# Kernel optimization log

Hardware: AMD Instinct MI355X
Metric: run time of the kernel (lower is better)

The kernel has to match this reference:

```python
import jax, jax.numpy as jnp
import numpy as np

B, S, D, H = 2, 2048, 1024, 16
HD = D // H  # head_dim = 64


def setup_inputs() -> dict:
    key = jax.random.key(0)
    ks = jax.random.split(key, 9)
    sc = 1.0 / np.sqrt(D)
    return {
        "X": jax.random.normal(ks[0], (B, S, D), jnp.float32),
        "Wq": jax.random.normal(ks[1], (D, D), jnp.float32) * sc,
        "bq": jnp.zeros((D,), jnp.float32),
        "Wk": jax.random.normal(ks[2], (D, D), jnp.float32) * sc,
        "bk": jnp.zeros((D,), jnp.float32),
        "Wv": jax.random.normal(ks[3], (D, D), jnp.float32) * sc,
        "bv": jnp.zeros((D,), jnp.float32),
        "Wo": jax.random.normal(ks[4], (D, D), jnp.float32) * sc,
        "bo": jnp.zeros((D,), jnp.float32),
    }


def reference(X, Wq, bq, Wk, bk, Wv, bv, Wo, bo):
    b, s, d = X.shape
    q = (X @ Wq + bq).reshape(b, s, H, HD).transpose(0, 2, 1, 3)  # [B,H,S,HD]
    k = (X @ Wk + bk).reshape(b, s, H, HD).transpose(0, 2, 1, 3)
    v = (X @ Wv + bv).reshape(b, s, H, HD).transpose(0, 2, 1, 3)
    score = jnp.einsum("bhqd,bhkd->bhqk", q, k) / jnp.sqrt(jnp.float32(HD))
    causal = jnp.tril(jnp.ones((s, s), bool))  # [S,S]
    score = jnp.where(causal[None, None], score, -jnp.inf)
    attn = jax.nn.softmax(score, axis=-1)
    out = jnp.einsum("bhqk,bhkd->bhqd", attn, v)  # [B,H,S,HD]
    out = out.transpose(0, 2, 1, 3).reshape(b, s, d)
    return out @ Wo + bo
```

## Files before the change

kernel.cpp:

```cpp
#include <hip/hip_runtime.h>
#include <hip/hip_bf16.h>
#include <math.h>

#define B_SZ 2
#define S_SZ 2048
#define D_SZ 1024
#define H_SZ 16
#define HD_SZ 64
constexpr int M_ROWS = B_SZ * S_SZ;

typedef __bf16 bf16x8 __attribute__((ext_vector_type(8)));
typedef __bf16 bf16x4 __attribute__((ext_vector_type(4)));
typedef float f32x4 __attribute__((ext_vector_type(4)));

#define GLOAD_LDS16(gsrc, ldst)                                              \
  __builtin_amdgcn_global_load_lds(                                          \
      (const __attribute__((address_space(1))) void*)(gsrc),                 \
      (__attribute__((address_space(3))) void*)(ldst), 16, 0, 0)

__global__ __launch_bounds__(256) void cvt_bf16(const float* __restrict__ in,
                                                __bf16* __restrict__ out,
                                                int n8) {
  const int i = blockIdx.x * 256 + threadIdx.x;
  if (i >= n8) return;
  const float4 a = *reinterpret_cast<const float4*>(&in[i * 8]);
  const float4 b = *reinterpret_cast<const float4*>(&in[i * 8 + 4]);
  bf16x8 o;
  o[0] = (__bf16)a.x; o[1] = (__bf16)a.y; o[2] = (__bf16)a.z; o[3] = (__bf16)a.w;
  o[4] = (__bf16)b.x; o[5] = (__bf16)b.y; o[6] = (__bf16)b.z; o[7] = (__bf16)b.w;
  *reinterpret_cast<bf16x8*>(&out[i * 8]) = o;
}

__global__ __launch_bounds__(256) void cvt_w_t_all(const float* __restrict__ W0,
                                                   const float* __restrict__ W1,
                                                   const float* __restrict__ W2,
                                                   const float* __restrict__ W3,
                                                   __bf16* __restrict__ Wt) {
  __shared__ float Ts[32][33];
  const int z = blockIdx.z;
  const float* W = z == 0 ? W0 : (z == 1 ? W1 : (z == 2 ? W2 : W3));
  __bf16* out = Wt + (size_t)z * 1024 * 1024;
  const int k0 = blockIdx.x * 32, n0 = blockIdx.y * 32;
  const int tr = threadIdx.x >> 3;
  const int tc = (threadIdx.x & 7) * 4;
  const float4 v = *reinterpret_cast<const float4*>(&W[(size_t)(k0 + tr) * 1024 + n0 + tc]);
  Ts[tr][tc + 0] = v.x;
  Ts[tr][tc + 1] = v.y;
  Ts[tr][tc + 2] = v.z;
  Ts[tr][tc + 3] = v.w;
  __syncthreads();
  bf16x4 o;
#pragma unroll
  for (int j = 0; j < 4; ++j) o[j] = (__bf16)Ts[tc + j][tr];
  *reinterpret_cast<bf16x4*>(&out[(size_t)(n0 + tr) * 1024 + k0 + tc]) = o;
}

__global__ __launch_bounds__(256) void transpose_v(const __bf16* __restrict__ V,
                                                   __bf16* __restrict__ Vt) {
  constexpr int TST = 66;
  __shared__ __bf16 T[64 * TST];
  const int bh = blockIdx.y;
  const int s0 = blockIdx.x * 64;
  const size_t base = (size_t)bh * S_SZ * HD_SZ;
  const int tid = threadIdx.x;
  for (int i = tid; i < 512; i += 256) {
    const int r = i >> 3, c = (i & 7) * 8;
    *reinterpret_cast<bf16x8*>(&T[r * TST + c]) =
        *reinterpret_cast<const bf16x8*>(&V[base + (size_t)(s0 + r) * 64 + c]);
  }
  __syncthreads();
  const size_t obase = (size_t)bh * HD_SZ * S_SZ;
  for (int i = tid; i < 512; i += 256) {
    const int d = i >> 3, c = (i & 7) * 8;
    bf16x8 o;
#pragma unroll
    for (int j = 0; j < 8; ++j) o[j] = T[(c + j) * TST + d];
    *reinterpret_cast<bf16x8*>(&Vt[obase + (size_t)d * S_SZ + s0 + c]) = o;
  }
}

template <int MODE>
__global__ __launch_bounds__(256) void gemm_mfma(
    const __bf16* __restrict__ Ab, const __bf16* __restrict__ Bt,
    const float* __restrict__ bias0, const float* __restrict__ bias1,
    const float* __restrict__ bias2, float* __restrict__ C0,
    __bf16* __restrict__ Q0, __bf16* __restrict__ K0, __bf16* __restrict__ V0,
    int M, int N, int K) {
  __shared__ __bf16 As[2][128 * 32];
  __shared__ __bf16 Bs[2][128 * 32];

  const int tid = threadIdx.x;
  const int lane = tid & 63;
  const int w = tid >> 6;
  const int lr = lane & 15, lg = lane >> 4;
  const int wr = w >> 1, wc = w & 1;
  const int bm = blockIdx.x * 128;
  const int bn = blockIdx.y * 128;

  const int r0 = tid >> 2, c0 = (tid & 3) * 8;
  const int r1 = (tid + 256) >> 2, c1 = ((tid + 256) & 3) * 8;
  const __bf16* aS0 = &Ab[(size_t)(bm + r0) * K + c0];
  const __bf16* aS1 = &Ab[(size_t)(bm + r1) * K + c1];
  const __bf16* bS0 = &Bt[(size_t)(bn + r0) * K + c0];
  const __bf16* bS1 = &Bt[(size_t)(bn + r1) * K + c1];

  f32x4 acc[4][4] = {};

  auto STAGE = [&](int buf) {
    GLOAD_LDS16(aS0, &As[buf][w * 512]);
    GLOAD_LDS16(aS1, &As[buf][2048 + w * 512]);
    GLOAD_LDS16(bS0, &Bs[buf][w * 512]);
    GLOAD_LDS16(bS1, &Bs[buf][2048 + w * 512]);
    aS0 += 32; aS1 += 32; bS0 += 32; bS1 += 32;
  };

  STAGE(0);
  asm volatile("s_waitcnt vmcnt(0)" ::: "memory");
  __builtin_amdgcn_s_barrier();
  __builtin_amdgcn_sched_barrier(0);
  int cur = 0;

  for (int k0 = 0; k0 < K; k0 += 32) {
    const bool has_next = (k0 + 32 < K);
    if (has_next) STAGE(cur ^ 1);
    if (k0) {
      if (has_next)
        asm volatile("s_waitcnt vmcnt(4)" ::: "memory");
      else
        asm volatile("s_waitcnt vmcnt(0)" ::: "memory");
      __builtin_amdgcn_s_barrier();
      __builtin_amdgcn_sched_barrier(0);
    }

    bf16x8 af[4], bfr[4];
#pragma unroll
    for (int i = 0; i < 4; ++i)
      af[i] = *reinterpret_cast<const bf16x8*>(&As[cur][(wr * 64 + i * 16 + lr) * 32 + lg * 8]);
#pragma unroll
    for (int j = 0; j < 4; ++j)
      bfr[j] = *reinterpret_cast<const bf16x8*>(&Bs[cur][(wc * 64 + j * 16 + lr) * 32 + lg * 8]);
    __builtin_amdgcn_s_setprio(1);
#pragma unroll
    for (int i = 0; i < 4; ++i)
#pragma unroll
      for (int j = 0; j < 4; ++j)
        acc[i][j] = __builtin_amdgcn_mfma_f32_16x16x32_bf16(af[i], bfr[j], acc[i][j], 0, 0, 0);
    __builtin_amdgcn_s_setprio(0);
    __builtin_amdgcn_sched_barrier(0);
    __builtin_amdgcn_s_barrier();
    cur ^= 1;
  }

  if (MODE == 0) {
#pragma unroll
    for (int j = 0; j < 4; ++j) {
      const int n = bn + wc * 64 + j * 16 + lr;
      const float bs = bias0[n];
#pragma unroll
      for (int i = 0; i < 4; ++i) {
        const int mrow = bm + wr * 64 + i * 16 + lg * 4;
#pragma unroll
        for (int r = 0; r < 4; ++r)
          C0[(size_t)(mrow + r) * N + n] = acc[i][j][r] + bs;
      }
    }
  } else {
    const int which = bn >> 10;
    __bf16* dst = which == 0 ? Q0 : (which == 1 ? K0 : V0);
    const float* bp = which == 0 ? bias0 : (which == 1 ? bias1 : bias2);
    const float scale = which == 0 ? 0.18033688011112042f : 1.0f;
#pragma unroll
    for (int j = 0; j < 4; ++j) {
      const int nn = (bn & 1023) + wc * 64 + j * 16 + lr;
      const int hh = nn >> 6, hd = nn & 63;
      const float bs = bp[nn];
#pragma unroll
      for (int i = 0; i < 4; ++i) {
        const int mrow = bm + wr * 64 + i * 16 + lg * 4;
#pragma unroll
        for (int r = 0; r < 4; ++r) {
          const int m = mrow + r;
          const int bb = m >> 11, ss = m & (S_SZ - 1);
          dst[(((size_t)(bb * H_SZ + hh)) * S_SZ + ss) * HD_SZ + hd] =
              (__bf16)((acc[i][j][r] + bs) * scale);
        }
      }
    }
  }
}

__global__ __launch_bounds__(256) void attn_mfma(const __bf16* __restrict__ Q,
                                                 const __bf16* __restrict__ Kg,
                                                 const __bf16* __restrict__ Vtg,
                                                 __bf16* __restrict__ Aout) {
  constexpr int PST = 40;
  __shared__ __bf16 Ks[2][64 * 64];
  __shared__ __bf16 Vts[2][64 * 64];
  __shared__ __bf16 Ps[4][16 * PST];

  const int tid = threadIdx.x;
  const int lane = tid & 63;
  const int w = tid >> 6;
  const int lr = lane & 15;
  const int lg = lane >> 4;

  const int flat = blockIdx.x;
  const int qb = 31 - (flat >> 5);
  const int hb = flat & 31;
  const int h = hb >> 1, b = hb & 1;
  const size_t base = (size_t)(b * H_SZ + h) * S_SZ * HD_SZ;
  const int q0 = qb * 64 + w * 16;

  bf16x8 aq[2];
#pragma unroll
  for (int hh = 0; hh < 2; ++hh)
    aq[hh] = *reinterpret_cast<const bf16x8*>(
        &Q[base + (size_t)(q0 + lr) * 64 + hh * 32 + lg * 8]);

  const int srow = lane >> 3;
  const int schunk = (lane & 7) ^ srow;

  bf16x8 ones8;
#pragma unroll
  for (int j = 0; j < 8; ++j) ones8[j] = (__bf16)1.0f;

  f32x4 oacc[4] = {};
  f32x4 oacc_l = {};

  const int ntiles = qb + 1;

  const int rbA = w * 16, rbB = w * 16 + 8;
  const __bf16* kS0 = &Kg[base + (size_t)(rbA + srow) * 64 + schunk * 8];
  const __bf16* kS1 = &Kg[base + (size_t)(rbB + srow) * 64 + schunk * 8];
  const __bf16* vS0 = &Vtg[base + (size_t)(rbA + srow) * S_SZ + schunk * 8];
  const __bf16* vS1 = &Vtg[base + (size_t)(rbB + srow) * S_SZ + schunk * 8];

  auto ISSUE = [&](int buf) {
    GLOAD_LDS16(kS0, &Ks[buf][rbA * 64]);
    GLOAD_LDS16(kS1, &Ks[buf][rbB * 64]);
    GLOAD_LDS16(vS0, &Vts[buf][rbA * 64]);
    GLOAD_LDS16(vS1, &Vts[buf][rbB * 64]);
  };

  ISSUE(0);
  asm volatile("s_waitcnt vmcnt(0)" ::: "memory");
  __builtin_amdgcn_s_barrier();
  __builtin_amdgcn_sched_barrier(0);
  int cur = 0;

  for (int t0 = 0; t0 < ntiles; ++t0) {
    const bool has_next = (t0 + 1 < ntiles);
    if (has_next) {
      kS0 += 64 * 64; kS1 += 64 * 64;
      vS0 += 64;      vS1 += 64;
      ISSUE(cur ^ 1);
    }
    if (t0) {
      if (has_next)
        asm volatile("s_waitcnt vmcnt(4)" ::: "memory");
      else
        asm volatile("s_waitcnt vmcnt(0)" ::: "memory");
      __builtin_amdgcn_s_barrier();
      __builtin_amdgcn_sched_barrier(0);
    }

    f32x4 s[4];
    __builtin_amdgcn_s_setprio(1);
#pragma unroll
    for (int t = 0; t < 4; ++t) {
      const int row = t * 16 + lr;
      const bf16x8 k0f = *reinterpret_cast<const bf16x8*>(
          &Ks[cur][row * 64 + ((lg ^ (lr & 7)) * 8)]);
      const bf16x8 k1f = *reinterpret_cast<const bf16x8*>(
          &Ks[cur][row * 64 + (((4 | lg) ^ (lr & 7)) * 8)]);
      f32x4 z = (f32x4){0.f, 0.f, 0.f, 0.f};
      z = __builtin_amdgcn_mfma_f32_16x16x32_bf16(aq[0], k0f, z, 0, 0, 0);
      z = __builtin_amdgcn_mfma_f32_16x16x32_bf16(aq[1], k1f, z, 0, 0, 0);
      s[t] = z;
    }
    __builtin_amdgcn_s_setprio(0);

    if (t0 == qb) {
#pragma unroll
      for (int t = 0; t < 4; ++t) {
        const int key = t0 * 64 + t * 16 + lr;
#pragma unroll
        for (int r = 0; r < 4; ++r) {
          const int qrow = q0 + lg * 4 + r;
          if (key > qrow) s[t][r] = -INFINITY;
        }
      }
    }

#pragma unroll
    for (int t = 0; t < 4; ++t)
#pragma unroll
      for (int r = 0; r < 4; ++r)
        s[t][r] = __builtin_amdgcn_exp2f(s[t][r]);

    __bf16* const psw = &Ps[w][0];
#pragma unroll
    for (int kh = 0; kh < 2; ++kh) {
#pragma unroll
      for (int t2 = 0; t2 < 2; ++t2)
#pragma unroll
        for (int r = 0; r < 4; ++r)
          psw[(lg * 4 + r) * PST + t2 * 16 + lr] = (__bf16)s[kh * 2 + t2][r];
      asm volatile("s_waitcnt lgkmcnt(0)" ::: "memory");
      __builtin_amdgcn_sched_barrier(0);
      const bf16x8 pa = *reinterpret_cast<const bf16x8*>(&psw[lr * PST + lg * 8]);
      __builtin_amdgcn_s_setprio(1);
#pragma unroll
      for (int dc = 0; dc < 4; ++dc) {
        const int row = dc * 16 + lr;
        const bf16x8 vf = *reinterpret_cast<const bf16x8*>(
            &Vts[cur][row * 64 + (((kh * 4 + lg) ^ (lr & 7)) * 8)]);
        oacc[dc] = __builtin_amdgcn_mfma_f32_16x16x32_bf16(pa, vf, oacc[dc], 0, 0, 0);
      }
      oacc_l = __builtin_amdgcn_mfma_f32_16x16x32_bf16(pa, ones8, oacc_l, 0, 0, 0);
      __builtin_amdgcn_s_setprio(0);
      __builtin_amdgcn_sched_barrier(0);
    }

    __builtin_amdgcn_sched_barrier(0);
    __builtin_amdgcn_s_barrier();
    cur ^= 1;
  }

#pragma unroll
  for (int r = 0; r < 4; ++r) {
    const float inv = 1.f / oacc_l[r];
    const int qg = q0 + lg * 4 + r;
#pragma unroll
    for (int dc = 0; dc < 4; ++dc)
      Aout[(size_t)(b * S_SZ + qg) * D_SZ + h * 64 + dc * 16 + lr] =
          (__bf16)(oacc[dc][r] * inv);
  }
}

extern "C" void kernel_launch(void* const* d_in, const int* in_sizes, int n_in,
                              void* d_out, int out_size, void* d_ws,
                              size_t ws_size, hipStream_t stream) {
  const float* X = (const float*)d_in[0];
  const float* Wq = (const float*)d_in[1];
  const float* bq = (const float*)d_in[2];
  const float* Wk = (const float*)d_in[3];
  const float* bk = (const float*)d_in[4];
  const float* Wv = (const float*)d_in[5];
  const float* bv = (const float*)d_in[6];
  const float* Wo = (const float*)d_in[7];
  const float* bo = (const float*)d_in[8];
  float* out = (float*)d_out;

  const size_t elems = (size_t)M_ROWS * D_SZ;
  const size_t welems = (size_t)D_SZ * D_SZ;
  __bf16* Xb = (__bf16*)d_ws;
  __bf16* Wt = Xb + elems;
  __bf16* Q = Wt + 4 * welems;
  __bf16* K = Q + elems;
  __bf16* V = K + elems;
  __bf16* Vt = V + elems;
  __bf16* Ahb = Vt + elems;

  cvt_bf16<<<(int)(elems / 8 / 256), 256, 0, stream>>>(X, Xb, (int)(elems / 8));
  cvt_w_t_all<<<dim3(32, 32, 4), 256, 0, stream>>>(Wq, Wk, Wv, Wo, Wt);

  gemm_mfma<1><<<dim3(M_ROWS / 128, 3072 / 128), 256, 0, stream>>>(
      Xb, Wt, bq, bk, bv, nullptr, Q, K, V, M_ROWS, 3072, D_SZ);

  transpose_v<<<dim3(32, 32), 256, 0, stream>>>(V, Vt);

  attn_mfma<<<dim3(1024), 256, 0, stream>>>(Q, K, Vt, Ahb);

  gemm_mfma<0><<<dim3(M_ROWS / 128, D_SZ / 128), 256, 0, stream>>>(
      Ahb, Wt + 3 * welems, bo, nullptr, nullptr, out, nullptr, nullptr,
      nullptr, M_ROWS, D_SZ, D_SZ);
}
```

Baseline: 116.0 us.

## Stage GEMM and attention epilogues through LDS, narrow output GEMM tile, rebalance attention blocks

The QKV GEMM epilogue now writes bf16 results into an LDS buffer and stores them as 16-byte vectors into the head-major Q/K/V layout, replacing scattered 2-byte stores. The attention kernel writes all P tiles for a step at once with a wider LDS stride, waits for LDS once per step instead of per half, and stages its output through LDS for vectorized stores. Attention blocks are interleaved so long and short causal rows mix across dispatch order. The output projection GEMM uses 64-wide N tiles, giving twice as many blocks for better CU occupancy at the cost of lower reuse per block.

```diff
diff --git a/kernel.cpp b/kernel.cpp
--- a/kernel.cpp
+++ b/kernel.cpp
@@ -79,15 +79,17 @@
   }
 }
 
-template <int MODE>
+template <int MODE, int BN>
 __global__ __launch_bounds__(256) void gemm_mfma(
     const __bf16* __restrict__ Ab, const __bf16* __restrict__ Bt,
     const float* __restrict__ bias0, const float* __restrict__ bias1,
     const float* __restrict__ bias2, float* __restrict__ C0,
     __bf16* __restrict__ Q0, __bf16* __restrict__ K0, __bf16* __restrict__ V0,
     int M, int N, int K) {
+  constexpr int NJ = BN / 32;
   __shared__ __bf16 As[2][128 * 32];
-  __shared__ __bf16 Bs[2][128 * 32];
+  __shared__ __bf16 Bs[2][BN * 32];
+  __shared__ __bf16 Ep[(MODE == 1) ? 32 * 132 : 4];
 
   const int tid = threadIdx.x;
   const int lane = tid & 63;
@@ -95,7 +97,7 @@
   const int lr = lane & 15, lg = lane >> 4;
   const int wr = w >> 1, wc = w & 1;
   const int bm = blockIdx.x * 128;
-  const int bn = blockIdx.y * 128;
+  const int bn = blockIdx.y * BN;
 
   const int r0 = tid >> 2, c0 = (tid & 3) * 8;
   const int r1 = (tid + 256) >> 2, c1 = ((tid + 256) & 3) * 8;
@@ -104,14 +106,15 @@
   const __bf16* bS0 = &Bt[(size_t)(bn + r0) * K + c0];
   const __bf16* bS1 = &Bt[(size_t)(bn + r1) * K + c1];
 
-  f32x4 acc[4][4] = {};
+  f32x4 acc[4][NJ] = {};
 
   auto STAGE = [&](int buf) {
     GLOAD_LDS16(aS0, &As[buf][w * 512]);
     GLOAD_LDS16(aS1, &As[buf][2048 + w * 512]);
     GLOAD_LDS16(bS0, &Bs[buf][w * 512]);
-    GLOAD_LDS16(bS1, &Bs[buf][2048 + w * 512]);
-    aS0 += 32; aS1 += 32; bS0 += 32; bS1 += 32;
+    if constexpr (BN == 128) GLOAD_LDS16(bS1, &Bs[buf][2048 + w * 512]);
+    aS0 += 32; aS1 += 32; bS0 += 32;
+    if constexpr (BN == 128) bS1 += 32;
   };
 
   STAGE(0);
@@ -124,26 +127,30 @@
     const bool has_next = (k0 + 32 < K);
     if (has_next) STAGE(cur ^ 1);
     if (k0) {
-      if (has_next)
-        asm volatile("s_waitcnt vmcnt(4)" ::: "memory");
-      else
+      if (has_next) {
+        if constexpr (BN == 128)
+          asm volatile("s_waitcnt vmcnt(4)" ::: "memory");
+        else
+          asm volatile("s_waitcnt vmcnt(3)" ::: "memory");
+      } else {
         asm volatile("s_waitcnt vmcnt(0)" ::: "memory");
+      }
       __builtin_amdgcn_s_barrier();
       __builtin_amdgcn_sched_barrier(0);
     }
 
-    bf16x8 af[4], bfr[4];
+    bf16x8 af[4], bfr[NJ];
 #pragma unroll
     for (int i = 0; i < 4; ++i)
       af[i] = *reinterpret_cast<const bf16x8*>(&As[cur][(wr * 64 + i * 16 + lr) * 32 + lg * 8]);
 #pragma unroll
-    for (int j = 0; j < 4; ++j)
-      bfr[j] = *reinterpret_cast<const bf16x8*>(&Bs[cur][(wc * 64 + j * 16 + lr) * 32 + lg * 8]);
+    for (int j = 0; j < NJ; ++j)
+      bfr[j] = *reinterpret_cast<const bf16x8*>(&Bs[cur][(wc * (BN / 2) + j * 16 + lr) * 32 + lg * 8]);
     __builtin_amdgcn_s_setprio(1);
 #pragma unroll
     for (int i = 0; i < 4; ++i)
 #pragma unroll
-      for (int j = 0; j < 4; ++j)
+      for (int j = 0; j < NJ; ++j)
         acc[i][j] = __builtin_amdgcn_mfma_f32_16x16x32_bf16(af[i], bfr[j], acc[i][j], 0, 0, 0);
     __builtin_amdgcn_s_setprio(0);
     __builtin_amdgcn_sched_barrier(0);
@@ -153,8 +160,8 @@
 
   if (MODE == 0) {
 #pragma unroll
-    for (int j = 0; j < 4; ++j) {
-      const int n = bn + wc * 64 + j * 16 + lr;
+    for (int j = 0; j < NJ; ++j) {
+      const int n = bn + wc * (BN / 2) + j * 16 + lr;
       const float bs = bias0[n];
 #pragma unroll
       for (int i = 0; i < 4; ++i) {
@@ -169,21 +176,35 @@
     __bf16* dst = which == 0 ? Q0 : (which == 1 ? K0 : V0);
     const float* bp = which == 0 ? bias0 : (which == 1 ? bias1 : bias2);
     const float scale = which == 0 ? 0.18033688011112042f : 1.0f;
-#pragma unroll
-    for (int j = 0; j < 4; ++j) {
-      const int nn = (bn & 1023) + wc * 64 + j * 16 + lr;
-      const int hh = nn >> 6, hd = nn & 63;
-      const float bs = bp[nn];
-#pragma unroll
-      for (int i = 0; i < 4; ++i) {
-        const int mrow = bm + wr * 64 + i * 16 + lg * 4;
-#pragma unroll
-        for (int r = 0; r < 4; ++r) {
-          const int m = mrow + r;
-          const int bb = m >> 11, ss = m & (S_SZ - 1);
-          dst[(((size_t)(bb * H_SZ + hh)) * S_SZ + ss) * HD_SZ + hd] =
-              (__bf16)((acc[i][j][r] + bs) * scale);
-        }
+    float bias4[4];
+#pragma unroll
+    for (int j = 0; j < 4; ++j)
+      bias4[j] = bp[(bn & 1023) + wc * 64 + j * 16 + lr];
+
+#pragma unroll
+    for (int i = 0; i < 4; ++i) {
+      __syncthreads();
+#pragma unroll
+      for (int j = 0; j < 4; ++j) {
+        const int colw = wc * 64 + j * 16 + lr;
+#pragma unroll
+        for (int r = 0; r < 4; ++r)
+          Ep[(wr * 16 + lg * 4 + r) * 132 + colw] =
+              (__bf16)((acc[i][j][r] + bias4[j]) * scale);
+      }
+      __syncthreads();
+#pragma unroll
+      for (int u = 0; u < 2; ++u) {
+        const int c = tid + u * 256;
+        const int er = c >> 4;
+        const int off = (c & 15) * 8;
+        const int m = bm + (er >> 4) * 64 + i * 16 + (er & 15);
+        const int nn = (bn & 1023) + off;
+        const int hh = nn >> 6, hd = nn & 63;
+        const int bb = m >> 11, ss = m & (S_SZ - 1);
+        *reinterpret_cast<bf16x8*>(
+            &dst[(((size_t)(bb * H_SZ + hh)) * S_SZ + ss) * HD_SZ + hd]) =
+            *reinterpret_cast<const bf16x8*>(&Ep[er * 132 + off]);
       }
     }
   }
@@ -193,7 +214,7 @@
                                                  const __bf16* __restrict__ Kg,
                                                  const __bf16* __restrict__ Vtg,
                                                  __bf16* __restrict__ Aout) {
-  constexpr int PST = 40;
+  constexpr int PST = 76;
   __shared__ __bf16 Ks[2][64 * 64];
   __shared__ __bf16 Vts[2][64 * 64];
   __shared__ __bf16 Ps[4][16 * PST];
@@ -205,7 +226,8 @@
   const int lg = lane >> 4;
 
   const int flat = blockIdx.x;
-  const int qb = 31 - (flat >> 5);
+  const int g = flat >> 5;
+  const int qb = (g < 16) ? (31 - g) : (g - 16);
   const int hb = flat & 31;
   const int h = hb >> 1, b = hb & 1;
   const size_t base = (size_t)(b * H_SZ + h) * S_SZ * HD_SZ;
@@ -296,20 +318,16 @@
     for (int t = 0; t < 4; ++t)
 #pragma unroll
       for (int r = 0; r < 4; ++r)
-        s[t][r] = __builtin_amdgcn_exp2f(s[t][r]);
-
-    __bf16* const psw = &Ps[w][0];
+        Ps[w][(lg * 4 + r) * PST + t * 16 + lr] =
+            (__bf16)__builtin_amdgcn_exp2f(s[t][r]);
+    asm volatile("s_waitcnt lgkmcnt(0)" ::: "memory");
+    __builtin_amdgcn_sched_barrier(0);
+
+    __builtin_amdgcn_s_setprio(1);
 #pragma unroll
     for (int kh = 0; kh < 2; ++kh) {
-#pragma unroll
-      for (int t2 = 0; t2 < 2; ++t2)
-#pragma unroll
-        for (int r = 0; r < 4; ++r)
-          psw[(lg * 4 + r) * PST + t2 * 16 + lr] = (__bf16)s[kh * 2 + t2][r];
-      asm volatile("s_waitcnt lgkmcnt(0)" ::: "memory");
-      __builtin_amdgcn_sched_barrier(0);
-      const bf16x8 pa = *reinterpret_cast<const bf16x8*>(&psw[lr * PST + lg * 8]);
-      __builtin_amdgcn_s_setprio(1);
+      const bf16x8 pa = *reinterpret_cast<const bf16x8*>(
+          &Ps[w][lr * PST + kh * 32 + lg * 8]);
 #pragma unroll
       for (int dc = 0; dc < 4; ++dc) {
         const int row = dc * 16 + lr;
@@ -318,9 +336,8 @@
         oacc[dc] = __builtin_amdgcn_mfma_f32_16x16x32_bf16(pa, vf, oacc[dc], 0, 0, 0);
       }
       oacc_l = __builtin_amdgcn_mfma_f32_16x16x32_bf16(pa, ones8, oacc_l, 0, 0, 0);
-      __builtin_amdgcn_s_setprio(0);
-      __builtin_amdgcn_sched_barrier(0);
-    }
+    }
+    __builtin_amdgcn_s_setprio(0);
 
     __builtin_amdgcn_sched_barrier(0);
     __builtin_amdgcn_s_barrier();
@@ -330,11 +347,21 @@
 #pragma unroll
   for (int r = 0; r < 4; ++r) {
     const float inv = 1.f / oacc_l[r];
-    const int qg = q0 + lg * 4 + r;
 #pragma unroll
     for (int dc = 0; dc < 4; ++dc)
-      Aout[(size_t)(b * S_SZ + qg) * D_SZ + h * 64 + dc * 16 + lr] =
-          (__bf16)(oacc[dc][r] * inv);
+      Ps[w][(lg * 4 + r) * PST + dc * 16 + lr] = (__bf16)(oacc[dc][r] * inv);
+  }
+  asm volatile("s_waitcnt lgkmcnt(0)" ::: "memory");
+  __builtin_amdgcn_sched_barrier(0);
+#pragma unroll
+  for (int u = 0; u < 2; ++u) {
+    const int c = lane + u * 64;
+    const int row = c >> 3;
+    const int off = (c & 7) * 8;
+    const int qg = q0 + row;
+    *reinterpret_cast<bf16x8*>(
+        &Aout[(size_t)(b * S_SZ + qg) * D_SZ + h * 64 + off]) =
+        *reinterpret_cast<const bf16x8*>(&Ps[w][row * PST + off]);
   }
 }
 
@@ -365,14 +392,14 @@
   cvt_bf16<<<(int)(elems / 8 / 256), 256, 0, stream>>>(X, Xb, (int)(elems / 8));
   cvt_w_t_all<<<dim3(32, 32, 4), 256, 0, stream>>>(Wq, Wk, Wv, Wo, Wt);
 
-  gemm_mfma<1><<<dim3(M_ROWS / 128, 3072 / 128), 256, 0, stream>>>(
+  gemm_mfma<1, 128><<<dim3(M_ROWS / 128, 3072 / 128), 256, 0, stream>>>(
       Xb, Wt, bq, bk, bv, nullptr, Q, K, V, M_ROWS, 3072, D_SZ);
 
   transpose_v<<<dim3(32, 32), 256, 0, stream>>>(V, Vt);
 
   attn_mfma<<<dim3(1024), 256, 0, stream>>>(Q, K, Vt, Ahb);
 
-  gemm_mfma<0><<<dim3(M_ROWS / 128, D_SZ / 128), 256, 0, stream>>>(
+  gemm_mfma<0, 64><<<dim3(M_ROWS / 128, D_SZ / 64), 256, 0, stream>>>(
       Ahb, Wt + 3 * welems, bo, nullptr, nullptr, out, nullptr, nullptr,
       nullptr, M_ROWS, D_SZ, D_SZ);
 }
```

Result: faster. 110.5 us (-4.8%).
